# Optimization experiments

Hardware: AMD Instinct MI355X
Metric: run time of the kernel (lower is better)

Reference implementation:

```python
import jax, jax.numpy as jnp
import numpy as np

N, D, HID, E, XD = 50000, 128, 64, 800000, 3

def _p(key, shape, scale=0.05):
    return jax.random.normal(key, shape, dtype=jnp.float32) * scale

def setup_inputs() -> dict:
    key = jax.random.key(0)
    ks = jax.random.split(key, 16)
    h = jax.random.normal(ks[0], (N, D), dtype=jnp.float32)
    x = jax.random.normal(ks[1], (N, XD), dtype=jnp.float32)
    edge_index = jax.random.randint(ks[2], (2, E), 0, N, dtype=jnp.int32)
    return {
        'h': h, 'x': x, 'edge_index': edge_index,
        'We1': _p(ks[3], (HID, 2 * D + 1)), 'be1': jnp.zeros((HID,), jnp.float32),
        'We2': _p(ks[4], (HID, HID)), 'be2': jnp.zeros((HID,), jnp.float32),
        'ln_g': jnp.ones((HID,), jnp.float32), 'ln_b': jnp.zeros((HID,), jnp.float32),
        'Wh1': _p(ks[5], (HID, D + HID)), 'bh1': jnp.zeros((HID,), jnp.float32),
        'Wh2': _p(ks[6], (D, HID)), 'bh2': jnp.zeros((D,), jnp.float32),
        'Wx': _p(ks[7], (1, HID)), 'bx': jnp.zeros((1,), jnp.float32),
        'Wg': _p(ks[8], (1, HID)), 'bg': jnp.zeros((1,), jnp.float32),
    }

def reference(h, x, edge_index, We1, be1, We2, be2, ln_g, ln_b,
              Wh1, bh1, Wh2, bh2, Wx, bx, Wg, bg):
    src, dst = edge_index[0], edge_index[1]
    n_nodes = h.shape[0]
    r = x[src] - x[dst]                          # (E, 3)
    d_sq = jnp.sum(r * r, axis=-1, keepdims=True)  # (E, 1)
    r_n = r / (jnp.sqrt(d_sq) + 1e-8)
    # phi_e: Linear -> SiLU -> Linear -> SiLU -> LayerNorm
    e_in = jnp.concatenate([h[src], h[dst], d_sq], axis=-1)  # (E, 2d+1)
    z = jax.nn.silu(e_in @ We1.T + be1)
    z = jax.nn.silu(z @ We2.T + be2)
    mu = jnp.mean(z, axis=-1, keepdims=True)
    var = jnp.mean((z - mu) ** 2, axis=-1, keepdims=True)
    m = (z - mu) * jax.lax.rsqrt(var + 1e-5) * ln_g + ln_b   # (E, hid)
    # gate and gated messages
    alpha = jax.nn.sigmoid(m @ Wg.T + bg)                     # (E, 1)
    m_gated = m * alpha
    agg_h = jax.ops.segment_sum(m_gated, dst, num_segments=n_nodes)  # (N, hid)
    # coordinate update (tanh_coords=True)
    cw = jnp.tanh(m_gated @ Wx.T + bx)                        # (E, 1)
    agg_x = jax.ops.segment_sum(r_n * cw, dst, num_segments=n_nodes)  # (N, 3)
    # coords_agg='mean': divide by in-degree clamped to 1
    deg = jax.ops.segment_sum(jnp.ones((src.shape[0], 1), h.dtype), dst,
                              num_segments=n_nodes)
    agg_x = agg_x / jnp.maximum(deg, 1.0)
    # phi_h residual update
    hh = jax.nn.silu(jnp.concatenate([h, agg_h], axis=-1) @ Wh1.T + bh1)
    h_new = h + (hh @ Wh2.T + bh2)
    x_new = x + agg_x
    return (h_new, x_new)
```

## Files before the change

### kernel.cpp

```cpp
#include <hip/hip_runtime.h>
#include <math.h>

#define HID 64
#define DF  128
#define HB  256

typedef __attribute__((ext_vector_type(8))) short short8v;
typedef __attribute__((ext_vector_type(4))) float float4v;

__device__ __forceinline__ float silu_f(float v) {
    return v * __builtin_amdgcn_rcpf(1.0f + __expf(-v));
}

__device__ __forceinline__ unsigned short f2bf(float f) {
    unsigned u = __float_as_uint(f);
    u += 0x7FFFu + ((u >> 16) & 1u);
    return (unsigned short)(u >> 16);
}

__device__ __forceinline__ short8v pack_bf16(float4 a, float4 b) {
    short8v r;
    r[0] = (short)f2bf(a.x); r[1] = (short)f2bf(a.y);
    r[2] = (short)f2bf(a.z); r[3] = (short)f2bf(a.w);
    r[4] = (short)f2bf(b.x); r[5] = (short)f2bf(b.y);
    r[6] = (short)f2bf(b.z); r[7] = (short)f2bf(b.w);
    return r;
}

__device__ __forceinline__ void wredsum4(float& a, float& b, float& c, float& d) {
#pragma unroll
    for (int t = 1; t < 64; t <<= 1) {
        a += __shfl_xor(a, t, 64);
        b += __shfl_xor(b, t, 64);
        c += __shfl_xor(c, t, 64);
        d += __shfl_xor(d, t, 64);
    }
}

__global__ void prep_weights(const float* __restrict__ We1, const float* __restrict__ We2,
                             const float* __restrict__ Wh1, const float* __restrict__ Wh2,
                             float* __restrict__ Wt1, float* __restrict__ Wt2,
                             unsigned short* __restrict__ WbfA,
                             unsigned short* __restrict__ WpB1,
                             unsigned short* __restrict__ WpH1,
                             unsigned short* __restrict__ WpH2) {
    int i = blockIdx.x * 256 + threadIdx.x;
    if (i < 257 * 64) {
        int k = i >> 6, f = i & 63;
        Wt1[i] = We1[f * 257 + k];
        return;
    }
    int j = i - 257 * 64;
    if (j < 64 * 64) {
        int k = j >> 6, f = j & 63;
        Wt2[j] = We2[f * 64 + k];
        return;
    }
    j -= 64 * 64;
    if (j < 4096) {
        int jj = j & 7, lane = (j >> 3) & 63, kc = (j >> 9) & 1, t = (j >> 10) & 3;
        int f = t * 16 + (lane & 15);
        int k = kc * 32 + ((lane >> 4) * 8) + jj;
        WbfA[j] = f2bf(We2[f * 64 + k]);
        return;
    }
    j -= 4096;
    if (j < 16384) {
        int jj = j & 7, lane = (j >> 3) & 63, kc = (j >> 9) & 3, ft = j >> 11;
        int f = ft * 16 + (lane & 15);
        int k = kc * 32 + ((lane >> 4) * 8) + jj;
        float v = (f < 64) ? We1[f * 257 + k] : We1[(f - 64) * 257 + 128 + k];
        WpB1[j] = f2bf(v);
        return;
    }
    j -= 16384;
    if (j < 12288) {
        int jj = j & 7, lane = (j >> 3) & 63, idx = j >> 9;
        int kc = idx % 6, ft = idx / 6;
        int f = ft * 16 + (lane & 15);
        int k = kc * 32 + ((lane >> 4) * 8) + jj;
        WpH1[j] = f2bf(Wh1[f * 192 + k]);
        return;
    }
    j -= 12288;
    if (j < 8192) {
        int jj = j & 7, lane = (j >> 3) & 63, idx = j >> 9;
        int kc = idx & 1, ft = idx >> 1;
        int c = ft * 16 + (lane & 15);
        int k = kc * 32 + ((lane >> 4) * 8) + jj;
        WpH2[j] = f2bf(Wh2[c * 64 + k]);
        return;
    }
}

__global__ __launch_bounds__(256) void count_kernel(const int* __restrict__ dst,
                                                    int* __restrict__ cnt,
                                                    int* __restrict__ rank, int E) {
    int e = blockIdx.x * 256 + threadIdx.x;
    if (e >= E) return;
    int r = atomicAdd(&cnt[dst[e]], 1);
    if (rank) rank[e] = r;
}

__global__ __launch_bounds__(1024) void scan1(const int* __restrict__ cnt,
                                              int* __restrict__ off,
                                              int* __restrict__ bsum, int N) {
    __shared__ int sm[1024];
    int tid = threadIdx.x;
    int i = blockIdx.x * 1024 + tid;
    int v = (i < N) ? cnt[i] : 0;
    sm[tid] = v;
    __syncthreads();
    for (int ofs = 1; ofs < 1024; ofs <<= 1) {
        int t = (tid >= ofs) ? sm[tid - ofs] : 0;
        __syncthreads();
        sm[tid] += t;
        __syncthreads();
    }
    if (i < N) off[i] = sm[tid] - v;
    if (tid == 1023) bsum[blockIdx.x] = sm[1023];
}

__global__ __launch_bounds__(256) void scan3(int* __restrict__ off,
                                             const int* __restrict__ bsum,
                                             int Nb, int N, int E) {
    __shared__ int pref[64];
    if (threadIdx.x == 0) {
        int s = 0;
        for (int b = 0; b < Nb; ++b) { pref[b] = s; s += bsum[b]; }
    }
    __syncthreads();
    int i = blockIdx.x * 256 + threadIdx.x;
    if (i > N) return;
    if (i == N) off[N] = E;
    else off[i] += pref[i >> 10];
}

__global__ __launch_bounds__(256) void scatter_src(const int* __restrict__ dst,
                                                   const int* __restrict__ srcI,
                                                   const int* __restrict__ rank,
                                                   const int* __restrict__ off,
                                                   int* __restrict__ csr_src, int E) {
    int e = blockIdx.x * 256 + threadIdx.x;
    if (e >= E) return;
    csr_src[off[dst[e]] + rank[e]] = srcI[e];
}

__global__ __launch_bounds__(HB) void hist_local(const int* __restrict__ cnt,
                                                 int* __restrict__ lrank,
                                                 int* __restrict__ blockcnt, int N) {
    __shared__ int lh[64];
    int tid = threadIdx.x;
    if (tid < 64) lh[tid] = 0;
    __syncthreads();
    int n = blockIdx.x * HB + tid;
    if (n < N) {
        int b = min(cnt[n], 63);
        lrank[n] = atomicAdd(&lh[b], 1);
    }
    __syncthreads();
    if (tid < 64) blockcnt[blockIdx.x * 64 + tid] = lh[tid];
}

__global__ __launch_bounds__(1024) void hist_tot(const int* __restrict__ blockcnt,
                                                 int* __restrict__ bucketbase, int nblk) {
    __shared__ int part[16][64];
    int b = threadIdx.x & 63, j = threadIdx.x >> 6;
    int s = 0;
    for (int k = j; k < nblk; k += 16) s += blockcnt[k * 64 + b];
    part[j][b] = s;
    __syncthreads();
    if (threadIdx.x < 64) {
        int t = 0;
#pragma unroll
        for (int jj = 1; jj < 16; ++jj) t += part[jj][threadIdx.x];
        part[0][threadIdx.x] += t;
    }
    __syncthreads();
    if (threadIdx.x == 0) {
        int base = 0;
        for (int bb = 0; bb < 64; ++bb) {
            int t = part[0][bb];
            bucketbase[bb] = base;
            base += t;
        }
    }
}

__global__ __launch_bounds__(64) void hist_scan2(int* __restrict__ blockcnt,
                                                 const int* __restrict__ bucketbase,
                                                 int nblk) {
    int b = blockIdx.x;
    int lane = threadIdx.x;
    int carry = bucketbase[b];
    for (int chunk = 0; chunk * 64 < nblk; ++chunk) {
        int k = chunk * 64 + lane;
        int c = (k < nblk) ? blockcnt[k * 64 + b] : 0;
        int v = c;
#pragma unroll
        for (int ofs = 1; ofs < 64; ofs <<= 1) {
            int t = __shfl_up(v, ofs, 64);
            if (lane >= ofs) v += t;
        }
        if (k < nblk) blockcnt[k * 64 + b] = carry + v - c;
        carry += __shfl(v, 63, 64);
    }
}

__global__ __launch_bounds__(HB) void degscatter2(const int* __restrict__ cnt,
                                                  const int* __restrict__ lrank,
                                                  const int* __restrict__ blockcnt,
                                                  int* __restrict__ nodeorder, int N) {
    int n = blockIdx.x * HB + threadIdx.x;
    if (n >= N) return;
    int b = min(cnt[n], 63);
    int pos = blockcnt[(n / HB) * 64 + b] + lrank[n];
    nodeorder[N - 1 - pos] = n;
}

__global__ __launch_bounds__(256) void node_pre(
    const float* __restrict__ h, const unsigned short* __restrict__ WpB1,
    const float* __restrict__ be1, const float* __restrict__ xin,
    float* __restrict__ Ps, float* __restrict__ Pd,
    float4* __restrict__ x4, int N) {
    const int lane = threadIdx.x & 63;
    const int wslot = threadIdx.x >> 6;
    {
        int n = blockIdx.x * 64 + threadIdx.x;
        if (threadIdx.x < 64 && n < N)
            x4[n] = make_float4(xin[3 * n], xin[3 * n + 1], xin[3 * n + 2], 0.f);
    }
    const int tile = (blockIdx.x * 4 + wslot) * 16;
    if (tile >= N) return;
    const int r15 = lane & 15, kg = lane >> 4;
    const int arow = min(tile + r15, N - 1);
    const float* hr = h + (size_t)arow * DF + kg * 8;
    short8v A[4];
#pragma unroll
    for (int kc = 0; kc < 4; ++kc) {
        float4 q0 = *(const float4*)(hr + kc * 32);
        float4 q1 = *(const float4*)(hr + kc * 32 + 4);
        A[kc] = pack_bf16(q0, q1);
    }
#pragma unroll
    for (int ft = 0; ft < 8; ++ft) {
        float4v c = (float4v){0.f, 0.f, 0.f, 0.f};
#pragma unroll
        for (int kc = 0; kc < 4; ++kc) {
            short8v B = *(const short8v*)&WpB1[(((ft * 4 + kc) * 64) + lane) * 8];
            c = __builtin_amdgcn_mfma_f32_16x16x32_bf16(A[kc], B, c, 0, 0, 0);
        }
        int f = ft * 16 + r15;
        float bias = (f >= 64) ? be1[f - 64] : 0.f;
#pragma unroll
        for (int r = 0; r < 4; ++r) {
            int n = tile + kg * 4 + r;
            if (n < N) {
                float v = c[r] + bias;
                if (f < 64) Ps[(size_t)n * 64 + f] = v;
                else        Pd[(size_t)n * 64 + (f - 64)] = v;
            }
        }
    }
}

__global__ __launch_bounds__(256) void gather_kernel(
    const int* __restrict__ csr_src, const int* __restrict__ off,
    const int* __restrict__ nodeorder, const float4* __restrict__ x4,
    const float* __restrict__ Ps, const float* __restrict__ Pd,
    const float* __restrict__ Wt1, const unsigned short* __restrict__ WbfA,
    const float* __restrict__ be2,
    const float* __restrict__ ln_g, const float* __restrict__ ln_b,
    const float* __restrict__ Wx, const float* __restrict__ bx,
    const float* __restrict__ Wg, const float* __restrict__ bg,
    float* __restrict__ agg_h, float* __restrict__ agg_x, int N) {
    const int lane = threadIdx.x & 63;
    const int wid = blockIdx.x * 4 + (threadIdx.x >> 6);
    const int e16 = lane & 15;
    const int hg = lane >> 4;
    const int k0 = hg * 8;
    const int p = e16 & 3;
    if (wid * 4 >= N) return;
    const int slot = wid * 4 + (e16 >> 2);

    short8v a[4][2];
#pragma unroll
    for (int t = 0; t < 4; ++t)
#pragma unroll
        for (int kc = 0; kc < 2; ++kc)
            a[t][kc] = *(const short8v*)&WbfA[(((t * 2 + kc) * 64) + lane) * 8];

    const float* colW = Wt1 + 256 * HID;
    float colWk[16];
#pragma unroll
    for (int j = 0; j < 8; ++j) {
        colWk[j] = colW[k0 + j];
        colWk[8 + j] = colW[k0 + 32 + j];
    }
    float be2r[16], cgr[16], cxr[16];
#pragma unroll
    for (int t = 0; t < 4; ++t)
#pragma unroll
        for (int r = 0; r < 4; ++r) {
            int f = t * 16 + hg * 4 + r;
            float g = ln_g[f];
            be2r[4 * t + r] = be2[f];
            cgr[4 * t + r] = g * Wg[f];
            cxr[4 * t + r] = g * Wx[f];
        }
    const float bgs = bg[0], bxs = bx[0];

    float Cg = ln_g[lane] * Wg[lane], Cx = ln_g[lane] * Wx[lane];
    float Cbg = ln_b[lane] * Wg[lane], Cbx = ln_b[lane] * Wx[lane];
    wredsum4(Cg, Cx, Cbg, Cbx);
    const float g0 = (lane < 16) ? 1.0f : 0.0f;

    const int nj = (slot < N) ? nodeorder[slot] : -1;
    int beg = 0, end = 0;
    if (nj >= 0) { beg = off[nj]; end = off[nj + 1]; }
    const float4 xdv = (nj >= 0) ? x4[nj] : make_float4(0.f, 0.f, 0.f, 0.f);
    float baseK[16];
    {
        const float4v* pd4 = (const float4v*)(Pd + (size_t)max(nj, 0) * HID + k0);
        float4v p0 = pd4[0], p1 = pd4[1], p2 = pd4[8], p3 = pd4[9];
#pragma unroll
        for (int j = 0; j < 4; ++j) {
            baseK[j] = p0[j];
            baseK[4 + j] = p1[j];
            baseK[8 + j] = p2[j];
            baseK[12 + j] = p3[j];
        }
    }

    int nb = (end - beg + 3) >> 2;
#pragma unroll
    for (int mk = 1; mk < 64; mk <<= 1) nb = max(nb, __shfl_xor(nb, mk, 64));
    nb = __builtin_amdgcn_readfirstlane(nb);

    float4v acc[4];
#pragma unroll
    for (int t = 0; t < 4; ++t) acc[t] = (float4v){0.f, 0.f, 0.f, 0.f};
    float ax0 = 0.f, ax1 = 0.f, ax2 = 0.f, Sa = 0.f, Smu = 0.f;

    for (int b = 0; b < nb; ++b) {
        int idx = beg + b * 4 + p;
        float validf = (idx < end) ? 1.0f : 0.0f;
        int ic = (idx < end) ? idx : (end > 0 ? end - 1 : 0);
        int s = csr_src[ic];
        float4 xs = x4[s];
        const float4v* ps4 = (const float4v*)(Ps + (size_t)s * HID + k0);
        float4v q0 = ps4[0], q1 = ps4[1], q2 = ps4[8], q3 = ps4[9];

        float r0 = xs.x - xdv.x, r1 = xs.y - xdv.y, r2 = xs.z - xdv.z;
        float dsq = r0 * r0 + r1 * r1 + r2 * r2;
        float inv = __builtin_amdgcn_rcpf(__builtin_amdgcn_sqrtf(dsq) + 1e-8f);

        short8v b0, b1;
#pragma unroll
        for (int j = 0; j < 4; ++j) {
            float z0 = q0[j] + baseK[j] + dsq * colWk[j];
            float z1 = q1[j] + baseK[4 + j] + dsq * colWk[4 + j];
            float z2 = q2[j] + baseK[8 + j] + dsq * colWk[8 + j];
            float z3 = q3[j] + baseK[12 + j] + dsq * colWk[12 + j];
            b0[j]     = (short)f2bf(silu_f(z0));
            b0[4 + j] = (short)f2bf(silu_f(z1));
            b1[j]     = (short)f2bf(silu_f(z2));
            b1[4 + j] = (short)f2bf(silu_f(z3));
        }

        float ms[16];
        float S1 = 0.f, S2 = 0.f, Sg = 0.f, Sx = 0.f;
#pragma unroll
        for (int t = 0; t < 4; ++t) {
            float4v c = (float4v){be2r[4 * t], be2r[4 * t + 1],
                                  be2r[4 * t + 2], be2r[4 * t + 3]};
            c = __builtin_amdgcn_mfma_f32_16x16x32_bf16(a[t][0], b0, c, 0, 0, 0);
            c = __builtin_amdgcn_mfma_f32_16x16x32_bf16(a[t][1], b1, c, 0, 0, 0);
#pragma unroll
            for (int r = 0; r < 4; ++r) {
                float v = c[r] * __builtin_amdgcn_rcpf(1.0f + __expf(-c[r]));
                ms[4 * t + r] = v;
                S1 += v;
                S2 = fmaf(v, v, S2);
                Sg = fmaf(v, cgr[4 * t + r], Sg);
                Sx = fmaf(v, cxr[4 * t + r], Sx);
            }
        }
#pragma unroll
        for (int mk = 16; mk < 64; mk <<= 1) {
            S1 += __shfl_xor(S1, mk, 64);
            S2 += __shfl_xor(S2, mk, 64);
            Sg += __shfl_xor(Sg, mk, 64);
            Sx += __shfl_xor(Sx, mk, 64);
        }

        float mu = S1 * (1.0f / HID);
        float var = S2 * (1.0f / HID) - mu * mu;
        float rstd = __builtin_amdgcn_rsqf(var + 1e-5f);
        float dg = fmaf(rstd, Sg - mu * Cg, Cbg);
        float dx = fmaf(rstd, Sx - mu * Cx, Cbx);
        float alpha = __builtin_amdgcn_rcpf(1.0f + __expf(-(dg + bgs))) * validf;
        float ta = __expf(2.0f * fmaf(alpha, dx, bxs));
        float cwv = 1.0f - 2.0f * __builtin_amdgcn_rcpf(ta + 1.0f);

        float u = rstd * alpha;
        Sa += alpha;
        Smu = fmaf(u, mu, Smu);
#pragma unroll
        for (int t = 0; t < 4; ++t) {
            float4v av = acc[t];
#pragma unroll
            for (int r = 0; r < 4; ++r) av[r] = fmaf(u, ms[4 * t + r], av[r]);
            acc[t] = av;
        }
        float rc = inv * cwv * validf * g0;
        ax0 = fmaf(r0, rc, ax0);
        ax1 = fmaf(r1, rc, ax1);
        ax2 = fmaf(r2, rc, ax2);
    }

#pragma unroll
    for (int t = 0; t < 4; ++t) {
        float4v av = acc[t];
#pragma unroll
        for (int r = 0; r < 4; ++r) {
            float v = av[r];
            v += __shfl_xor(v, 1, 64);
            v += __shfl_xor(v, 2, 64);
            av[r] = v;
        }
        acc[t] = av;
    }
    Sa  += __shfl_xor(Sa, 1, 64);  Sa  += __shfl_xor(Sa, 2, 64);
    Smu += __shfl_xor(Smu, 1, 64); Smu += __shfl_xor(Smu, 2, 64);
    ax0 += __shfl_xor(ax0, 1, 64); ax0 += __shfl_xor(ax0, 2, 64);
    ax1 += __shfl_xor(ax1, 1, 64); ax1 += __shfl_xor(ax1, 2, 64);
    ax2 += __shfl_xor(ax2, 1, 64); ax2 += __shfl_xor(ax2, 2, 64);

    if (p == 0 && nj >= 0) {
        float* dstp = agg_h + (size_t)nj * HID + hg * 4;
#pragma unroll
        for (int t = 0; t < 4; ++t) {
            int f = t * 16 + hg * 4;
            float4 o;
            o.x = fmaf(ln_g[f + 0], acc[t][0] - Smu, ln_b[f + 0] * Sa);
            o.y = fmaf(ln_g[f + 1], acc[t][1] - Smu, ln_b[f + 1] * Sa);
            o.z = fmaf(ln_g[f + 2], acc[t][2] - Smu, ln_b[f + 2] * Sa);
            o.w = fmaf(ln_g[f + 3], acc[t][3] - Smu, ln_b[f + 3] * Sa);
            *(float4*)(dstp + t * 16) = o;
        }
        if (hg == 0) {
            agg_x[nj * 3 + 0] = ax0;
            agg_x[nj * 3 + 1] = ax1;
            agg_x[nj * 3 + 2] = ax2;
        }
    }
}

__global__ __launch_bounds__(256) void edge_kernel_atomic(
    const int* __restrict__ src, const int* __restrict__ dst,
    const float* __restrict__ x,
    const float* __restrict__ Ps, const float* __restrict__ Pd,
    const float* __restrict__ Wt1, const float* __restrict__ Wt2,
    const float* __restrict__ be2,
    const float* __restrict__ ln_g, const float* __restrict__ ln_b,
    const float* __restrict__ Wx, const float* __restrict__ bx,
    const float* __restrict__ Wg, const float* __restrict__ bg,
    float* __restrict__ agg_h, float* __restrict__ agg_x, int E) {
    int e = blockIdx.x * 256 + threadIdx.x;
    if (e >= E) return;
    int s = src[e], d = dst[e];
    float r0 = x[s * 3] - x[d * 3], r1 = x[s * 3 + 1] - x[d * 3 + 1], r2 = x[s * 3 + 2] - x[d * 3 + 2];
    float dsq = r0 * r0 + r1 * r1 + r2 * r2;
    float inv = 1.0f / (sqrtf(dsq) + 1e-8f);
    float rn0 = r0 * inv, rn1 = r1 * inv, rn2 = r2 * inv;
    float z[HID];
    const float4* ps = (const float4*)(Ps + (size_t)s * HID);
    const float4* pd = (const float4*)(Pd + (size_t)d * HID);
    const float* colW = Wt1 + 256 * HID;
#pragma unroll
    for (int f4 = 0; f4 < HID / 4; ++f4) {
        float4 aa = ps[f4];
        float4 b = pd[f4];
        float av[4] = {aa.x, aa.y, aa.z, aa.w};
        float bv[4] = {b.x, b.y, b.z, b.w};
#pragma unroll
        for (int j = 0; j < 4; ++j) {
            int f = 4 * f4 + j;
            z[f] = silu_f(av[j] + bv[j] + dsq * colW[f]);
        }
    }
    float m[HID];
#pragma unroll
    for (int f = 0; f < HID; ++f) m[f] = be2[f];
#pragma unroll
    for (int k = 0; k < HID; ++k) {
        float zv = z[k];
#pragma unroll
        for (int f = 0; f < HID; ++f) m[f] = fmaf(zv, Wt2[k * HID + f], m[f]);
    }
#pragma unroll
    for (int f = 0; f < HID; ++f) m[f] = silu_f(m[f]);
    float mu = 0.f;
#pragma unroll
    for (int f = 0; f < HID; ++f) mu += m[f];
    mu *= (1.0f / HID);
    float var = 0.f;
#pragma unroll
    for (int f = 0; f < HID; ++f) {
        float t = m[f] - mu;
        var = fmaf(t, t, var);
    }
    var *= (1.0f / HID);
    float rstd = 1.0f / sqrtf(var + 1e-5f);
#pragma unroll
    for (int f = 0; f < HID; ++f) m[f] = (m[f] - mu) * rstd * ln_g[f] + ln_b[f];
    float dotg = 0.f, dotx = 0.f;
#pragma unroll
    for (int f = 0; f < HID; ++f) {
        dotg = fmaf(m[f], Wg[f], dotg);
        dotx = fmaf(m[f], Wx[f], dotx);
    }
    float alpha = 1.0f / (1.0f + __expf(-(dotg + bg[0])));
    float ta = __expf(2.0f * fmaf(alpha, dotx, bx[0]));
    float cw = 1.0f - 2.0f / (ta + 1.0f);
    float* ah = agg_h + (size_t)d * HID;
#pragma unroll
    for (int f = 0; f < HID; ++f) atomicAdd(&ah[f], m[f] * alpha);
    atomicAdd(&agg_x[d * 3 + 0], rn0 * cw);
    atomicAdd(&agg_x[d * 3 + 1], rn1 * cw);
    atomicAdd(&agg_x[d * 3 + 2], rn2 * cw);
}

__global__ __launch_bounds__(256) void node_kernel(
    const float* __restrict__ h, const float* __restrict__ xin,
    const float* __restrict__ agg_h, const float* __restrict__ agg_x,
    const int* __restrict__ degI,
    const unsigned short* __restrict__ WpH1, const unsigned short* __restrict__ WpH2,
    const float* __restrict__ bh1, const float* __restrict__ bh2,
    float* __restrict__ out, int N) {
    __shared__ float hhL[4][16][72];
    const int lane = threadIdx.x & 63;
    const int wslot = threadIdx.x >> 6;
    {
        int n = blockIdx.x * 64 + threadIdx.x;
        if (threadIdx.x < 64 && n < N) {
            float dv = (float)degI[n];
            float invd = 1.0f / fmaxf(dv, 1.0f);
            float* ox = out + (size_t)N * DF + (size_t)n * 3;
            ox[0] = xin[n * 3 + 0] + agg_x[n * 3 + 0] * invd;
            ox[1] = xin[n * 3 + 1] + agg_x[n * 3 + 1] * invd;
            ox[2] = xin[n * 3 + 2] + agg_x[n * 3 + 2] * invd;
        }
    }
    const int tile = (blockIdx.x * 4 + wslot) * 16;
    if (tile >= N) return;
    const int r15 = lane & 15, kg = lane >> 4;
    const int arow = min(tile + r15, N - 1);

    short8v A[6];
    const float* hr = h + (size_t)arow * DF + kg * 8;
#pragma unroll
    for (int kc = 0; kc < 4; ++kc) {
        float4 q0 = *(const float4*)(hr + kc * 32);
        float4 q1 = *(const float4*)(hr + kc * 32 + 4);
        A[kc] = pack_bf16(q0, q1);
    }
    const float* ar = agg_h + (size_t)arow * HID + kg * 8;
#pragma unroll
    for (int kc = 0; kc < 2; ++kc) {
        float4 q0 = *(const float4*)(ar + kc * 32);
        float4 q1 = *(const float4*)(ar + kc * 32 + 4);
        A[4 + kc] = pack_bf16(q0, q1);
    }

#pragma unroll
    for (int ft = 0; ft < 4; ++ft) {
        float4v c = (float4v){0.f, 0.f, 0.f, 0.f};
#pragma unroll
        for (int kc = 0; kc < 6; ++kc) {
            short8v B = *(const short8v*)&WpH1[(((ft * 6 + kc) * 64) + lane) * 8];
            c = __builtin_amdgcn_mfma_f32_16x16x32_bf16(A[kc], B, c, 0, 0, 0);
        }
        int f = ft * 16 + r15;
        float b1v = bh1[f];
#pragma unroll
        for (int r = 0; r < 4; ++r)
            hhL[wslot][kg * 4 + r][f] = silu_f(c[r] + b1v);
    }
    __builtin_amdgcn_wave_barrier();

    short8v HA[2];
#pragma unroll
    for (int kc = 0; kc < 2; ++kc) {
        float4 q0 = *(const float4*)&hhL[wslot][r15][kc * 32 + kg * 8];
        float4 q1 = *(const float4*)&hhL[wslot][r15][kc * 32 + kg * 8 + 4];
        HA[kc] = pack_bf16(q0, q1);
    }

#pragma unroll
    for (int ft = 0; ft < 8; ++ft) {
        float4v c = (float4v){0.f, 0.f, 0.f, 0.f};
#pragma unroll
        for (int kc = 0; kc < 2; ++kc) {
            short8v B = *(const short8v*)&WpH2[(((ft * 2 + kc) * 64) + lane) * 8];
            c = __builtin_amdgcn_mfma_f32_16x16x32_bf16(HA[kc], B, c, 0, 0, 0);
        }
        int cc = ft * 16 + r15;
        float b2 = bh2[cc];
#pragma unroll
        for (int r = 0; r < 4; ++r) {
            int n = tile + kg * 4 + r;
            if (n < N)
                out[(size_t)n * DF + cc] = h[(size_t)n * DF + cc] + c[r] + b2;
        }
    }
}

extern "C" void kernel_launch(void* const* d_in, const int* in_sizes, int n_in,
                              void* d_out, int out_size, void* d_ws, size_t ws_size,
                              hipStream_t stream) {
    const float* h    = (const float*)d_in[0];
    const float* x    = (const float*)d_in[1];
    const int*   ei   = (const int*)d_in[2];
    const float* We1  = (const float*)d_in[3];
    const float* be1  = (const float*)d_in[4];
    const float* We2  = (const float*)d_in[5];
    const float* be2  = (const float*)d_in[6];
    const float* ln_g = (const float*)d_in[7];
    const float* ln_b = (const float*)d_in[8];
    const float* Wh1  = (const float*)d_in[9];
    const float* bh1  = (const float*)d_in[10];
    const float* Wh2  = (const float*)d_in[11];
    const float* bh2  = (const float*)d_in[12];
    const float* Wx   = (const float*)d_in[13];
    const float* bx   = (const float*)d_in[14];
    const float* Wg   = (const float*)d_in[15];
    const float* bg   = (const float*)d_in[16];

    const int E = in_sizes[2] / 2;
    const int N = in_sizes[0] / DF;
    const int* src = ei;
    const int* dst = ei + E;

    char* base = (char*)d_ws;
    size_t o = 0;
    auto carve = [&](size_t bytes) -> void* {
        void* r = base + o;
        o = (o + bytes + 15) & ~(size_t)15;
        return r;
    };
    const int nblk = (N + HB - 1) / HB;
    float* agg_h = (float*)carve((size_t)N * HID * 4);
    float* agg_x = (float*)carve((size_t)N * 3 * 4);
    float* Wt1   = (float*)carve(257 * 64 * 4);
    float* Wt2   = (float*)carve(64 * 64 * 4);
    unsigned short* WbfA = (unsigned short*)carve(4096 * 2);
    unsigned short* WpB1 = (unsigned short*)carve(16384 * 2);
    unsigned short* WpH1 = (unsigned short*)carve(12288 * 2);
    unsigned short* WpH2 = (unsigned short*)carve(8192 * 2);
    int*   cnt   = (int*)carve((size_t)N * 4);
    int*   off   = (int*)carve(((size_t)N + 1) * 4);
    int*   bsum  = (int*)carve(256 * 4);
    int*   lrank = (int*)carve((size_t)N * 4);
    int*   blockcnt = (int*)carve((size_t)nblk * 64 * 4);
    int*   bucketbase = (int*)carve(64 * 4);
    int*   nodeorder = (int*)carve((size_t)N * 4);
    float4* x4   = (float4*)carve((size_t)N * 16);
    int*   rank  = (int*)carve((size_t)E * 4);
    int*   csr_src = (int*)carve((size_t)E * 4);
    size_t need_full = o;

    float* Ps = (float*)d_out;
    float* Pd = Ps + (size_t)N * HID;

    const int gE  = (E + 255) / 256;
    const int Nb  = (N + 1023) / 1024;
    const int tiles = (N + 15) / 16;
    const int gT  = (tiles + 3) / 4;

    hipMemsetAsync(cnt, 0, (size_t)N * 4, stream);
    prep_weights<<<(61504 + 255) / 256, 256, 0, stream>>>(
        We1, We2, Wh1, Wh2, Wt1, Wt2, WbfA, WpB1, WpH1, WpH2);
    node_pre<<<gT, 256, 0, stream>>>(h, WpB1, be1, x, Ps, Pd, x4, N);

    if (ws_size >= need_full) {
        count_kernel<<<gE, 256, 0, stream>>>(dst, cnt, rank, E);
        scan1<<<Nb, 1024, 0, stream>>>(cnt, off, bsum, N);
        scan3<<<(N + 256) / 256, 256, 0, stream>>>(off, bsum, Nb, N, E);
        scatter_src<<<gE, 256, 0, stream>>>(dst, src, rank, off, csr_src, E);
        hist_local<<<nblk, HB, 0, stream>>>(cnt, lrank, blockcnt, N);
        hist_tot<<<1, 1024, 0, stream>>>(blockcnt, bucketbase, nblk);
        hist_scan2<<<64, 64, 0, stream>>>(blockcnt, bucketbase, nblk);
        degscatter2<<<nblk, HB, 0, stream>>>(cnt, lrank, blockcnt, nodeorder, N);
        const int quads = (N + 3) / 4;
        gather_kernel<<<(quads + 3) / 4, 256, 0, stream>>>(
            csr_src, off, nodeorder, x4, Ps, Pd, Wt1, WbfA, be2,
            ln_g, ln_b, Wx, bx, Wg, bg, agg_h, agg_x, N);
    } else {
        hipMemsetAsync(agg_h, 0, (size_t)N * 67 * 4, stream);
        count_kernel<<<gE, 256, 0, stream>>>(dst, cnt, nullptr, E);
        edge_kernel_atomic<<<gE, 256, 0, stream>>>(src, dst, x, Ps, Pd, Wt1, Wt2,
                                                   be2, ln_g, ln_b, Wx, bx,
                                                   Wg, bg, agg_h, agg_x, E);
    }

    node_kernel<<<gT, 256, 0, stream>>>(h, x, agg_h, agg_x, cnt,
                                        WpH1, WpH2, bh1, bh2, (float*)d_out, N);
}
```

Baseline: 197.9 us.

## Pack bf16 via hardware cvt, prefetch CSR src, fold memset and x-update into kernels

Replaces the software round-to-nearest bf16 conversion with the packed v_cvt_pk_bf16_f32 instruction. Prefetches the next edge's source index in the gather loop to hide latency. Folds the cnt memset into prep_weights and computes the final coordinate update directly in the gather kernel, so node_kernel skips that work and agg_x is never written. This trims instruction count and a launch, but it relies on the gfx950 conversion instruction and on the gather path's own degree count.

Result: faster. 188.6 us (-4.7%).

```diff
diff --git a/kernel.cpp b/kernel.cpp
--- a/kernel.cpp
+++ b/kernel.cpp
@@ -7,6 +7,7 @@
 
 typedef __attribute__((ext_vector_type(8))) short short8v;
 typedef __attribute__((ext_vector_type(4))) float float4v;
+typedef __attribute__((ext_vector_type(4))) unsigned int uint4v;
 
 __device__ __forceinline__ float silu_f(float v) {
     return v * __builtin_amdgcn_rcpf(1.0f + __expf(-v));
@@ -18,13 +19,26 @@
     return (unsigned short)(u >> 16);
 }
 
+__device__ __forceinline__ unsigned cvt2(float lo, float hi) {
+    unsigned r;
+    asm("v_cvt_pk_bf16_f32 %0, %1, %2" : "=v"(r) : "v"(lo), "v"(hi));
+    return r;
+}
+
+__device__ __forceinline__ short8v pack8(float a0, float a1, float a2, float a3,
+                                         float a4, float a5, float a6, float a7) {
+    uint4v w;
+    w[0] = cvt2(a0, a1);
+    w[1] = cvt2(a2, a3);
+    w[2] = cvt2(a4, a5);
+    w[3] = cvt2(a6, a7);
+    union { uint4v u; short8v s; } cv;
+    cv.u = w;
+    return cv.s;
+}
+
 __device__ __forceinline__ short8v pack_bf16(float4 a, float4 b) {
-    short8v r;
-    r[0] = (short)f2bf(a.x); r[1] = (short)f2bf(a.y);
-    r[2] = (short)f2bf(a.z); r[3] = (short)f2bf(a.w);
-    r[4] = (short)f2bf(b.x); r[5] = (short)f2bf(b.y);
-    r[6] = (short)f2bf(b.z); r[7] = (short)f2bf(b.w);
-    return r;
+    return pack8(a.x, a.y, a.z, a.w, b.x, b.y, b.z, b.w);
 }
 
 __device__ __forceinline__ void wredsum4(float& a, float& b, float& c, float& d) {
@@ -37,14 +51,21 @@
     }
 }
 
+#define PREPW 61504
 __global__ void prep_weights(const float* __restrict__ We1, const float* __restrict__ We2,
                              const float* __restrict__ Wh1, const float* __restrict__ Wh2,
                              float* __restrict__ Wt1, float* __restrict__ Wt2,
                              unsigned short* __restrict__ WbfA,
                              unsigned short* __restrict__ WpB1,
                              unsigned short* __restrict__ WpH1,
-                             unsigned short* __restrict__ WpH2) {
+                             unsigned short* __restrict__ WpH2,
+                             int* __restrict__ cnt, int N) {
     int i = blockIdx.x * 256 + threadIdx.x;
+    if (i >= PREPW) {
+        int n = i - PREPW;
+        if (n < N) cnt[n] = 0;
+        return;
+    }
     if (i < 257 * 64) {
         int k = i >> 6, f = i & 63;
         Wt1[i] = We1[f * 257 + k];
@@ -273,7 +294,7 @@
     const float* __restrict__ ln_g, const float* __restrict__ ln_b,
     const float* __restrict__ Wx, const float* __restrict__ bx,
     const float* __restrict__ Wg, const float* __restrict__ bg,
-    float* __restrict__ agg_h, float* __restrict__ agg_x, int N) {
+    float* __restrict__ agg_h, float* __restrict__ xout, int N) {
     const int lane = threadIdx.x & 63;
     const int wid = blockIdx.x * 4 + (threadIdx.x >> 6);
     const int e16 = lane & 15;
@@ -342,11 +363,22 @@
     for (int t = 0; t < 4; ++t) acc[t] = (float4v){0.f, 0.f, 0.f, 0.f};
     float ax0 = 0.f, ax1 = 0.f, ax2 = 0.f, Sa = 0.f, Smu = 0.f;
 
+    int sC = 0;
+    if (nb > 0) {
+        int idx = beg + p;
+        int ic = (idx < end) ? idx : (end > 0 ? end - 1 : 0);
+        sC = csr_src[ic];
+    }
+
     for (int b = 0; b < nb; ++b) {
         int idx = beg + b * 4 + p;
         float validf = (idx < end) ? 1.0f : 0.0f;
-        int ic = (idx < end) ? idx : (end > 0 ? end - 1 : 0);
-        int s = csr_src[ic];
+        int s = sC;
+        if (b + 1 < nb) {
+            int idx2 = beg + (b + 1) * 4 + p;
+            int ic2 = (idx2 < end) ? idx2 : (end > 0 ? end - 1 : 0);
+            sC = csr_src[ic2];
+        }
         float4 xs = x4[s];
         const float4v* ps4 = (const float4v*)(Ps + (size_t)s * HID + k0);
         float4v q0 = ps4[0], q1 = ps4[1], q2 = ps4[8], q3 = ps4[9];
@@ -355,18 +387,16 @@
         float dsq = r0 * r0 + r1 * r1 + r2 * r2;
         float inv = __builtin_amdgcn_rcpf(__builtin_amdgcn_sqrtf(dsq) + 1e-8f);
 
-        short8v b0, b1;
+        float zb[16];
 #pragma unroll
         for (int j = 0; j < 4; ++j) {
-            float z0 = q0[j] + baseK[j] + dsq * colWk[j];
-            float z1 = q1[j] + baseK[4 + j] + dsq * colWk[4 + j];
-            float z2 = q2[j] + baseK[8 + j] + dsq * colWk[8 + j];
-            float z3 = q3[j] + baseK[12 + j] + dsq * colWk[12 + j];
-            b0[j]     = (short)f2bf(silu_f(z0));
-            b0[4 + j] = (short)f2bf(silu_f(z1));
-            b1[j]     = (short)f2bf(silu_f(z2));
-            b1[4 + j] = (short)f2bf(silu_f(z3));
-        }
+            zb[j]      = silu_f(q0[j] + baseK[j] + dsq * colWk[j]);
+            zb[4 + j]  = silu_f(q1[j] + baseK[4 + j] + dsq * colWk[4 + j]);
+            zb[8 + j]  = silu_f(q2[j] + baseK[8 + j] + dsq * colWk[8 + j]);
+            zb[12 + j] = silu_f(q3[j] + baseK[12 + j] + dsq * colWk[12 + j]);
+        }
+        short8v b0 = pack8(zb[0], zb[1], zb[2], zb[3], zb[4], zb[5], zb[6], zb[7]);
+        short8v b1 = pack8(zb[8], zb[9], zb[10], zb[11], zb[12], zb[13], zb[14], zb[15]);
 
         float ms[16];
         float S1 = 0.f, S2 = 0.f, Sg = 0.f, Sx = 0.f;
@@ -450,9 +480,11 @@
             *(float4*)(dstp + t * 16) = o;
         }
         if (hg == 0) {
-            agg_x[nj * 3 + 0] = ax0;
-            agg_x[nj * 3 + 1] = ax1;
-            agg_x[nj * 3 + 2] = ax2;
+            float invd = 1.0f / fmaxf((float)(end - beg), 1.0f);
+            float* ox = xout + (size_t)nj * 3;
+            ox[0] = xdv.x + ax0 * invd;
+            ox[1] = xdv.y + ax1 * invd;
+            ox[2] = xdv.z + ax2 * invd;
         }
     }
 }
@@ -538,11 +570,11 @@
     const int* __restrict__ degI,
     const unsigned short* __restrict__ WpH1, const unsigned short* __restrict__ WpH2,
     const float* __restrict__ bh1, const float* __restrict__ bh2,
-    float* __restrict__ out, int N) {
+    float* __restrict__ out, int N, int writeX) {
     __shared__ float hhL[4][16][72];
     const int lane = threadIdx.x & 63;
     const int wslot = threadIdx.x >> 6;
-    {
+    if (writeX) {
         int n = blockIdx.x * 64 + threadIdx.x;
         if (threadIdx.x < 64 && n < N) {
             float dv = (float)degI[n];
@@ -673,15 +705,15 @@
 
     float* Ps = (float*)d_out;
     float* Pd = Ps + (size_t)N * HID;
+    float* xout = (float*)d_out + (size_t)N * DF;
 
     const int gE  = (E + 255) / 256;
     const int Nb  = (N + 1023) / 1024;
     const int tiles = (N + 15) / 16;
     const int gT  = (tiles + 3) / 4;
 
-    hipMemsetAsync(cnt, 0, (size_t)N * 4, stream);
-    prep_weights<<<(61504 + 255) / 256, 256, 0, stream>>>(
-        We1, We2, Wh1, Wh2, Wt1, Wt2, WbfA, WpB1, WpH1, WpH2);
+    prep_weights<<<(PREPW + N + 255) / 256, 256, 0, stream>>>(
+        We1, We2, Wh1, Wh2, Wt1, Wt2, WbfA, WpB1, WpH1, WpH2, cnt, N);
     node_pre<<<gT, 256, 0, stream>>>(h, WpB1, be1, x, Ps, Pd, x4, N);
 
     if (ws_size >= need_full) {
@@ -696,15 +728,16 @@
         const int quads = (N + 3) / 4;
         gather_kernel<<<(quads + 3) / 4, 256, 0, stream>>>(
             csr_src, off, nodeorder, x4, Ps, Pd, Wt1, WbfA, be2,
-            ln_g, ln_b, Wx, bx, Wg, bg, agg_h, agg_x, N);
+            ln_g, ln_b, Wx, bx, Wg, bg, agg_h, xout, N);
+        node_kernel<<<gT, 256, 0, stream>>>(h, x, agg_h, agg_x, cnt,
+                                            WpH1, WpH2, bh1, bh2, (float*)d_out, N, 0);
     } else {
         hipMemsetAsync(agg_h, 0, (size_t)N * 67 * 4, stream);
         count_kernel<<<gE, 256, 0, stream>>>(dst, cnt, nullptr, E);
         edge_kernel_atomic<<<gE, 256, 0, stream>>>(src, dst, x, Ps, Pd, Wt1, Wt2,
                                                    be2, ln_g, ln_b, Wx, bx,
                                                    Wg, bg, agg_h, agg_x, E);
-    }
-
-    node_kernel<<<gT, 256, 0, stream>>>(h, x, agg_h, agg_x, cnt,
-                                        WpH1, WpH2, bh1, bh2, (float*)d_out, N);
-}
+        node_kernel<<<gT, 256, 0, stream>>>(h, x, agg_h, agg_x, cnt,
+                                            WpH1, WpH2, bh1, bh2, (float*)d_out, N, 1);
+    }
+}
```
